# Performance work log

Hardware: AMD Instinct MI355X
Metric: run time of the kernel (lower is better)

The kernel has to match this reference:

```python
import jax, jax.numpy as jnp
import numpy as np
from jax import lax
import math

B, C, L, H, K, NCONV = 64, 128, 400, 8, 7, 4  # batch, d_model, length, n_head, kernel, n_conv
DK = C // H
EPS = 1e-5


def setup_inputs() -> dict:
    key = jax.random.key(0)
    ks = jax.random.split(key, 16)
    inp = {
        'x': jax.random.normal(ks[0], (B, C, L), dtype=jnp.float32),
        'mask': jnp.ones((B, L), dtype=jnp.float32),
        'dw_w': jax.random.normal(ks[1], (NCONV, C, 1, K), dtype=jnp.float32) * 0.1,
        'dw_b': jnp.zeros((NCONV, C), dtype=jnp.float32),
        'pw_w': jax.random.normal(ks[2], (NCONV, C, C, 1), dtype=jnp.float32) * 0.05,
        'pw_b': jnp.zeros((NCONV, C), dtype=jnp.float32),
        'wq': jax.random.normal(ks[3], (C, C), dtype=jnp.float32) * 0.05,
        'bq': jnp.zeros((C,), dtype=jnp.float32),
        'wk': jax.random.normal(ks[4], (C, C), dtype=jnp.float32) * 0.05,
        'bk': jnp.zeros((C,), dtype=jnp.float32),
        'wv': jax.random.normal(ks[5], (C, C), dtype=jnp.float32) * 0.05,
        'bv': jnp.zeros((C,), dtype=jnp.float32),
        'wo': jax.random.normal(ks[6], (C, C), dtype=jnp.float32) * 0.05,
        'bo': jnp.zeros((C,), dtype=jnp.float32),
        'fc_w': jax.random.normal(ks[7], (C, C), dtype=jnp.float32) * 0.05,
        'fc_b': jnp.zeros((C,), dtype=jnp.float32),
        'ln_g': jnp.ones((C, L), dtype=jnpp.float32) if False else jnp.ones((C, L), dtype=jnp.float32),
        'ln_b': jnp.zeros((C, L), dtype=jnp.float32),
    }
    return inp


def _pos_encoding():
    i = jnp.arange(C, dtype=jnp.float32)
    even = (jnp.arange(C) % 2) == 0
    freqs = jnp.where(even, 10000.0 ** (-i / C), -(10000.0 ** ((1.0 - i) / C)))
    phases = jnp.where(even, 0.0, math.pi / 2.0)
    pos = jnp.arange(L, dtype=jnp.float32)
    return jnp.sin(pos[None, :] * freqs[:, None] + phases[:, None])  # (C, L)


def _layer_norm(o, g, b):
    # torch LayerNorm([d_model, length]): normalize each sample over (C, L) jointly
    mu = jnp.mean(o, axis=(1, 2), keepdims=True)
    var = jnp.mean((o - mu) ** 2, axis=(1, 2), keepdims=True)
    return (o - mu) * lax.rsqrt(var + EPS) * g[None] + b[None]


def _dwsep_conv(o, dw, db, pw, pb):
    # depthwise: groups=C, kernel (C,1,K), 'same' padding
    y = lax.conv_general_dilated(o, dw, window_strides=(1,), padding=[(K // 2, K // 2)],
                                 dimension_numbers=('NCH', 'OIH', 'NCH'), feature_group_count=C)
    y = y + db[None, :, None]
    # pointwise 1x1 conv
    y = jnp.einsum('oc,bcl->bol', pw[:, :, 0], y) + pb[None, :, None]
    return y


def _attention(o, mask, wq, bq, wk, bk, wv, bv, wo, bo):
    xt = jnp.transpose(o, (0, 2, 1))  # (B, L, C)
    q = (xt @ wq.T + bq).reshape(B, L, H, DK)
    k = (xt @ wk.T + bk).reshape(B, L, H, DK)
    v = (xt @ wv.T + bv).reshape(B, L, H, DK)
    atten = jnp.einsum('blhd,bmhd->bhlm', q, k) / math.sqrt(C)  # note: sqrt(d_model), faithful
    m = mask[:, None, None, :]  # (B,1,1,L)
    atten = atten * m + (1.0 - m) * -1e30
    atten = jax.nn.softmax(atten, axis=-1)
    out = jnp.einsum('bhlm,bmhd->blhd', atten, v).reshape(B, L, C)
    out = out @ wo.T + bo
    return jnp.transpose(out, (0, 2, 1))  # (B, C, L)


def reference(x, mask, dw_w, dw_b, pw_w, pw_b, wq, bq, wk, bk, wv, bv, wo, bo, fc_w, fc_b, ln_g, ln_b):
    out = x + _pos_encoding()[None]
    res = out
    out = _layer_norm(out, ln_g, ln_b)
    for i in range(NCONV):
        out = _dwsep_conv(out, dw_w[i], dw_b[i], pw_w[i], pw_b[i])
        out = jax.nn.relu(out)
        out = res + out
        res = out
        out = _layer_norm(out, ln_g, ln_b)
    out = _attention(out, mask, wq, bq, wk, bk, wv, bv, wo, bo)
    out = res + out
    res = out
    out = _layer_norm(out, ln_g, ln_b)
    out = jnp.einsum('bcl,ec->bel', out, fc_w) + fc_b[None, :, None]
    out = jax.nn.relu(out)
    out = res + out
    return out
```

## Files before the change

kernel.cpp:

```cpp
#include <hip/hip_runtime.h>
#include <math.h>

constexpr int BN = 64;
constexpr int CC = 128;
constexpr int LL = 400;
constexpr int DK = 16;
constexpr int KK = 7;
constexpr int CL = CC * LL;
constexpr int NBCL = BN * CL;
constexpr float EPSV = 1e-5f;
constexpr float INV_N = 1.0f / (float)CL;
constexpr float BIGL = 1.4427e30f;
constexpr int RW = 96;

typedef __attribute__((ext_vector_type(8))) short bf16x8;
typedef __attribute__((ext_vector_type(4))) float f32x4;

#if defined(__has_builtin)
#if __has_builtin(__builtin_amdgcn_exp2f)
#define EXP2F(x) __builtin_amdgcn_exp2f(x)
#endif
#endif
#ifndef EXP2F
#define EXP2F(x) exp2f(x)
#endif

__device__ __forceinline__ short f2bf(float f) {
  unsigned u = __builtin_bit_cast(unsigned, f);
  u = (u + 0x7fffu + ((u >> 16) & 1u)) >> 16;
  return (short)u;
}
__device__ __forceinline__ float bf2f(unsigned short u) {
  return __builtin_bit_cast(float, (unsigned)u << 16);
}
__device__ __forceinline__ unsigned pkbf(float hi, float lo) {
  return __builtin_amdgcn_perm(__builtin_bit_cast(unsigned, hi),
                               __builtin_bit_cast(unsigned, lo), 0x07060302u);
}

__device__ __forceinline__ void stats_pub(float* sx, int u, int bb, int jx,
                                          float* red, int tid) {
  if (tid == 0) {
    float a = 0.f, b2 = 0.f;
    #pragma unroll
    for (int w2 = 0; w2 < 8; w2++) { a += red[w2 * 2]; b2 += red[w2 * 2 + 1]; }
    float* base = sx + (u * 64 + bb) * 32;
    __hip_atomic_store(&base[jx * 2], a, __ATOMIC_RELAXED, __HIP_MEMORY_SCOPE_AGENT);
    __hip_atomic_store(&base[jx * 2 + 1], b2, __ATOMIC_RELAXED, __HIP_MEMORY_SCOPE_AGENT);
    asm volatile("s_waitcnt vmcnt(0)" ::: "memory");
    __hip_atomic_fetch_add(reinterpret_cast<int*>(&base[16]), 1,
                           __ATOMIC_RELAXED, __HIP_MEMORY_SCOPE_AGENT);
  }
}
__device__ __forceinline__ void stats_wait(float* sx, int u, int bb,
                                           float* red, int tid,
                                           float& mu, float& rstd) {
  if (tid == 0) {
    float* base = sx + (u * 64 + bb) * 32;
    while (__hip_atomic_load(reinterpret_cast<int*>(&base[16]),
                             __ATOMIC_RELAXED, __HIP_MEMORY_SCOPE_AGENT) < 7)
      __builtin_amdgcn_s_sleep(1);
    float s1 = 0.f, s2 = 0.f;
    #pragma unroll
    for (int k = 0; k < 7; k++) {
      s1 += __hip_atomic_load(&base[k * 2], __ATOMIC_RELAXED, __HIP_MEMORY_SCOPE_AGENT);
      s2 += __hip_atomic_load(&base[k * 2 + 1], __ATOMIC_RELAXED, __HIP_MEMORY_SCOPE_AGENT);
    }
    float m2 = s1 * INV_N;
    red[0] = m2;
    red[1] = rsqrtf(s2 * INV_N - m2 * m2 + EPSV);
  }
  __syncthreads();
  mu = red[0]; rstd = red[1];
  __syncthreads();
}

template<int XMODE>
__device__ __forceinline__ void stage_x(
    short* __restrict__ XsF, const unsigned short* __restrict__ Xb,
    int j0, const float* __restrict__ lng, const float* __restrict__ lnb,
    float mu, float rstd, int tid)
{
  for (int idx = tid; idx < 1024; idx += 512) {
    int c = idx >> 3;
    int l8 = (idx & 7) * 8;
    int col0 = j0 + l8;
    short hv[8];
    bool valid = col0 < LL;
    int col0c = valid ? col0 : 0;
    const unsigned short* xp = Xb + c * LL + col0c;
    const ushort4 u0 = *reinterpret_cast<const ushort4*>(&xp[0]);
    const ushort4 u1 = *reinterpret_cast<const ushort4*>(&xp[4]);
    unsigned short uu[8] = {u0.x, u0.y, u0.z, u0.w, u1.x, u1.y, u1.z, u1.w};
    if (XMODE == 1) {
      #pragma unroll
      for (int e = 0; e < 8; e++) hv[e] = valid ? (short)uu[e] : (short)0;
    } else {
      const float* gp = lng + c * LL + col0c;
      const float* bp = lnb + c * LL + col0c;
      const float4 g0 = *reinterpret_cast<const float4*>(&gp[0]);
      const float4 g1 = *reinterpret_cast<const float4*>(&gp[4]);
      const float4 b0 = *reinterpret_cast<const float4*>(&bp[0]);
      const float4 b1 = *reinterpret_cast<const float4*>(&bp[4]);
      float gg[8] = {g0.x, g0.y, g0.z, g0.w, g1.x, g1.y, g1.z, g1.w};
      float bbv[8] = {b0.x, b0.y, b0.z, b0.w, b1.x, b1.y, b1.z, b1.w};
      #pragma unroll
      for (int e = 0; e < 8; e++) {
        float v = (bf2f(uu[e]) - mu) * rstd * gg[e] + bbv[e];
        hv[e] = valid ? f2bf(v) : (short)0;
      }
    }
    int t = (l8 >> 4) * 4 + (c >> 5);
    int quad = (c >> 3) & 3;
    int j = c & 7;
    int base = t * 512 + quad * 128 + j;
    int colb = l8 & 15;
    #pragma unroll
    for (int e = 0; e < 8; e++) XsF[base + (colb + e) * 8] = hv[e];
  }
}

template<int XMODE, int OMODE, bool RELU, bool ADDRES, bool STATS>
__device__ __forceinline__ void gemm_gl(
    short* __restrict__ XsF, float* __restrict__ red,
    const float* __restrict__ Wsrc, const unsigned short* __restrict__ Xv,
    const float* __restrict__ bias, const unsigned short* __restrict__ resid,
    const float* __restrict__ lng, const float* __restrict__ lnb,
    float mu, float rstd, void* __restrict__ Yv)
{
  int tid = threadIdx.x;
  int bb = blockIdx.y;
  int j0 = blockIdx.x * 64;
  int w = tid >> 6, lane = tid & 63;
  int o = w * 16 + (lane & 15);
  int cb = (lane >> 4) * 8;
  bf16x8 af[4];
  #pragma unroll
  for (int kt = 0; kt < 4; kt++) {
    const float* wp = Wsrc + o * 128 + kt * 32 + cb;
    const float4 a0 = *reinterpret_cast<const float4*>(wp);
    const float4 a1 = *reinterpret_cast<const float4*>(wp + 4);
    bf16x8 v;
    v[0] = f2bf(a0.x); v[1] = f2bf(a0.y); v[2] = f2bf(a0.z); v[3] = f2bf(a0.w);
    v[4] = f2bf(a1.x); v[5] = f2bf(a1.y); v[6] = f2bf(a1.z); v[7] = f2bf(a1.w);
    af[kt] = v;
  }
  stage_x<XMODE>(XsF, Xv + (size_t)bb * CL, j0, lng, lnb, mu, rstd, tid);
  __syncthreads();
  int col = lane & 15, quad = lane >> 4;
  f32x4 acc[4];
  #pragma unroll
  for (int lf = 0; lf < 4; lf++) acc[lf] = (f32x4){0.f, 0.f, 0.f, 0.f};
  #pragma unroll
  for (int kt = 0; kt < 4; kt++) {
    #pragma unroll
    for (int lf = 0; lf < 4; lf++) {
      bf16x8 bx = *reinterpret_cast<const bf16x8*>(&XsF[(lf * 4 + kt) * 512 + lane * 8]);
      acc[lf] = __builtin_amdgcn_mfma_f32_16x16x32_bf16(af[kt], bx, acc[lf], 0, 0, 0);
    }
  }
  int obase = w * 16;
  float bv[4];
  #pragma unroll
  for (int r = 0; r < 4; r++) bv[r] = bias[obase + quad * 4 + r];
  float lsum = 0.f, lsq = 0.f;
  #pragma unroll
  for (int lf = 0; lf < 4; lf++) {
    if (j0 + lf * 16 < LL) {
      int l = j0 + lf * 16 + col;
      #pragma unroll
      for (int r = 0; r < 4; r++) {
        float v = acc[lf][r] + bv[r];
        if (RELU) v = fmaxf(v, 0.f);
        size_t oidx = (size_t)bb * CL + (size_t)(obase + quad * 4 + r) * LL + l;
        if (ADDRES) v += bf2f(resid[oidx]);
        if (OMODE == 1) {
          unsigned short hb = (unsigned short)f2bf(v);
          ((unsigned short*)Yv)[oidx] = hb;
          if (STATS) { float vf = bf2f(hb); lsum += vf; lsq += vf * vf; }
        } else {
          ((float*)Yv)[oidx] = v;
        }
      }
    }
  }
  if (STATS) {
    #pragma unroll
    for (int off = 32; off > 0; off >>= 1) {
      lsum += __shfl_down(lsum, off);
      lsq  += __shfl_down(lsq, off);
    }
    if (lane == 0) { red[w * 2] = lsum; red[w * 2 + 1] = lsq; }
    __syncthreads();
  }
}

__global__ __launch_bounds__(512, 4) void fused_main(
    const float* __restrict__ pw_w, const float* __restrict__ wq,
    const float* __restrict__ wk, const float* __restrict__ wvp,
    const float* __restrict__ pw_b, const float* __restrict__ dw_b,
    const float* __restrict__ mask, const float* __restrict__ x,
    const float* __restrict__ lng, const float* __restrict__ lnb,
    const float* __restrict__ dw_w,
    const float* __restrict__ bq, const float* __restrict__ bk,
    const float* __restrict__ bvp,
    float* __restrict__ sx, float* __restrict__ maddb,
    unsigned short* __restrict__ r0,
    unsigned short* __restrict__ qt, unsigned short* __restrict__ kt,
    unsigned short* __restrict__ vbf)
{
  __shared__ short Raw[128 * RW];
  __shared__ short XsF[24 * 512];
  __shared__ float red[16];
  int tid = threadIdx.x;
  int jx = blockIdx.x, bb = blockIdx.y;
  int gtid = (bb * 7 + jx) * 512 + tid;
  int g0tile = jx * 64 - 16;

  if (gtid < 26624) {
    int b = gtid / 416, m = gtid - b * 416;
    maddb[gtid] = (m < LL) ? (mask[b * LL + m] - 1.f) * BIGL : -BIGL;
  }

  {
    float s1 = 0.f, s2 = 0.f;
    for (int idx = tid; idx < 1536; idx += 512) {
      int c = idx & 127, grp = idx >> 7;
      int r = grp * 8;
      float fc2 = (float)c, freq, ph;
      if ((c & 1) == 0) { freq = powf(10000.f, -fc2 / (float)CC);        ph = 0.f; }
      else              { freq = -powf(10000.f, (1.f - fc2) / (float)CC); ph = 1.5707963267948966f; }
      #pragma unroll
      for (int e4 = 0; e4 < 2; e4++) {
        int g = g0tile + r + e4 * 4;
        bool valid4 = (g >= 0) && (g <= LL - 4);
        float4 xv = {0.f, 0.f, 0.f, 0.f};
        if (valid4)
          xv = *reinterpret_cast<const float4*>(&x[((size_t)bb * CC + c) * LL + g]);
        float xe[4] = {xv.x, xv.y, xv.z, xv.w};
        #pragma unroll
        for (int e = 0; e < 4; e++) {
          int rr = r + e4 * 4 + e;
          short hh = 0;
          if (valid4) {
            float p = sinf((float)(g + e) * freq + ph);
            hh = f2bf(xe[e] + p);
          }
          Raw[c * RW + rr] = hh;
          if (rr >= 16 && rr < 80 && (g + e) < LL) {
            float v = bf2f((unsigned short)hh);
            s1 += v; s2 += v * v;
          }
        }
      }
    }
    #pragma unroll
    for (int off = 32; off > 0; off >>= 1) {
      s1 += __shfl_down(s1, off);
      s2 += __shfl_down(s2, off);
    }
    int wv = tid >> 6, lane = tid & 63;
    if (lane == 0) { red[wv * 2] = s1; red[wv * 2 + 1] = s2; }
    __syncthreads();
    stats_pub(sx, 0, bb, jx, red, tid);
  }

  int w = tid >> 6, lane = tid & 63;
  int col = lane & 15, quad = lane >> 4;
  int obase = w * 16;
  int wo_ = w * 16 + (lane & 15);
  int cb = (lane >> 4) * 8;
  #pragma unroll 1
  for (int li = 0; li < 4; li++) {
    float mu, rstd;
    stats_wait(sx, li, bb, red, tid, mu, rstd);
    const float* dww = dw_w + li * CC * KK;
    const float* dwb = dw_b + li * CC;
    for (int idx = tid; idx < 1536; idx += 512) {
      int c = idx & 127, grp = idx >> 7;
      int l8 = grp * 8;
      float xn[16];
      const float* gp = lng + c * LL;
      const float* bp = lnb + c * LL;
      #pragma unroll
      for (int g4 = 0; g4 < 4; g4++) {
        int r0w = l8 - 4 + g4 * 4;
        int rc = r0w < 0 ? 0 : (r0w > RW - 4 ? RW - 4 : r0w);
        const ushort4 rv = *reinterpret_cast<const ushort4*>(&Raw[c * RW + rc]);
        unsigned short rr4[4] = {rv.x, rv.y, rv.z, rv.w};
        int gg = g0tile + r0w;
        int ggc = gg < 0 ? 0 : (gg > LL - 4 ? LL - 4 : gg);
        const float4 gv = *reinterpret_cast<const float4*>(&gp[ggc]);
        const float4 bv4 = *reinterpret_cast<const float4*>(&bp[ggc]);
        float ge[4] = {gv.x, gv.y, gv.z, gv.w};
        float be[4] = {bv4.x, bv4.y, bv4.z, bv4.w};
        #pragma unroll
        for (int e = 0; e < 4; e++) {
          int g = gg + e;
          float v = (bf2f(rr4[e]) - mu) * rstd * ge[e] + be[e];
          xn[g4 * 4 + e] = (g >= 0 && g < LL) ? v : 0.f;
        }
      }
      float w7[KK];
      #pragma unroll
      for (int j = 0; j < KK; j++) w7[j] = dww[c * KK + j];
      float dbc = dwb[c];
      short hv[8];
      #pragma unroll
      for (int e = 0; e < 8; e++) {
        float a = 0.f;
        #pragma unroll
        for (int jj = 0; jj < KK; jj++) a += w7[jj] * xn[e + jj + 1];
        hv[e] = f2bf(a + dbc);
      }
      int t = (l8 >> 4) * 4 + (c >> 5);
      int qd = (c >> 3) & 3;
      int j = c & 7;
      int base = t * 512 + qd * 128 + j;
      int colb = l8 & 15;
      #pragma unroll
      for (int e = 0; e < 8; e++) XsF[base + (colb + e) * 8] = hv[e];
    }
    __syncthreads();
    const float* Wsrc = pw_w + li * 16384;
    bf16x8 af[4];
    #pragma unroll
    for (int kt = 0; kt < 4; kt++) {
      const float* wp = Wsrc + wo_ * 128 + kt * 32 + cb;
      const float4 a0 = *reinterpret_cast<const float4*>(wp);
      const float4 a1 = *reinterpret_cast<const float4*>(wp + 4);
      bf16x8 v;
      v[0] = f2bf(a0.x); v[1] = f2bf(a0.y); v[2] = f2bf(a0.z); v[3] = f2bf(a0.w);
      v[4] = f2bf(a1.x); v[5] = f2bf(a1.y); v[6] = f2bf(a1.z); v[7] = f2bf(a1.w);
      af[kt] = v;
    }
    f32x4 acc[6];
    #pragma unroll
    for (int lf = 0; lf < 6; lf++) acc[lf] = (f32x4){0.f, 0.f, 0.f, 0.f};
    #pragma unroll
    for (int kt = 0; kt < 4; kt++) {
      #pragma unroll
      for (int lf = 0; lf < 6; lf++) {
        bf16x8 bx = *reinterpret_cast<const bf16x8*>(&XsF[(lf * 4 + kt) * 512 + lane * 8]);
        acc[lf] = __builtin_amdgcn_mfma_f32_16x16x32_bf16(af[kt], bx, acc[lf], 0, 0, 0);
      }
    }
    const float* bias = pw_b + li * CC;
    float bv[4];
    #pragma unroll
    for (int r = 0; r < 4; r++) bv[r] = bias[obase + quad * 4 + r];
    int m = 12 - 4 * li;
    float lsum = 0.f, lsq = 0.f;
    #pragma unroll
    for (int lf = 0; lf < 6; lf++) {
      int r = lf * 16 + col;
      int g = g0tile + r;
      bool vcol = (r >= 16 - m) && (r < 80 + m) && (g >= 0) && (g < LL);
      #pragma unroll
      for (int rr = 0; rr < 4; rr++) {
        if (vcol) {
          int o = obase + quad * 4 + rr;
          float v = acc[lf][rr] + bv[rr];
          v = fmaxf(v, 0.f);
          v += bf2f((unsigned short)Raw[o * RW + r]);
          unsigned short hb = (unsigned short)f2bf(v);
          Raw[o * RW + r] = (short)hb;
          if (li == 3)
            r0[(size_t)bb * CL + (size_t)o * LL + g] = hb;
          if (r >= 16 && r < 80) {
            float vf = bf2f(hb);
            lsum += vf; lsq += vf * vf;
          }
        }
      }
    }
    #pragma unroll
    for (int off = 32; off > 0; off >>= 1) {
      lsum += __shfl_down(lsum, off);
      lsq  += __shfl_down(lsq, off);
    }
    if (lane == 0) { red[w * 2] = lsum; red[w * 2 + 1] = lsq; }
    __syncthreads();
    stats_pub(sx, li + 1, bb, jx, red, tid);
  }

  {
    float mu, rstd;
    stats_wait(sx, 4, bb, red, tid, mu, rstd);
    int j0 = jx * 64;
    for (int idx = tid; idx < 1024; idx += 512) {
      int c = idx >> 3;
      int l8 = (idx & 7) * 8;
      bool valid = (j0 + l8) < LL;
      short hv[8];
      const ushort4 u0 = *reinterpret_cast<const ushort4*>(&Raw[c * RW + 16 + l8]);
      const ushort4 u1 = *reinterpret_cast<const ushort4*>(&Raw[c * RW + 20 + l8]);
      unsigned short uu[8] = {u0.x, u0.y, u0.z, u0.w, u1.x, u1.y, u1.z, u1.w};
      int col0c = valid ? (j0 + l8) : 0;
      const float* gp = lng + c * LL + col0c;
      const float* bp = lnb + c * LL + col0c;
      const float4 g0 = *reinterpret_cast<const float4*>(&gp[0]);
      const float4 g1 = *reinterpret_cast<const float4*>(&gp[4]);
      const float4 b0 = *reinterpret_cast<const float4*>(&bp[0]);
      const float4 b1 = *reinterpret_cast<const float4*>(&bp[4]);
      float gg[8] = {g0.x, g0.y, g0.z, g0.w, g1.x, g1.y, g1.z, g1.w};
      float bbv[8] = {b0.x, b0.y, b0.z, b0.w, b1.x, b1.y, b1.z, b1.w};
      #pragma unroll
      for (int e = 0; e < 8; e++) {
        float v = (bf2f(uu[e]) - mu) * rstd * gg[e] + bbv[e];
        hv[e] = valid ? f2bf(v) : (short)0;
      }
      int t = (l8 >> 4) * 4 + (c >> 5);
      int qd = (c >> 3) & 3;
      int j = c & 7;
      int base = t * 512 + qd * 128 + j;
      int colb = l8 & 15;
      #pragma unroll
      for (int e = 0; e < 8; e++) XsF[base + (colb + e) * 8] = hv[e];
    }
    __syncthreads();
    int j0q = jx * 64;
    #pragma unroll 1
    for (int mm = 0; mm < 3; mm++) {
      const float* Wsrc = (mm == 0) ? wq : (mm == 1) ? wk : wvp;
      const float* bias = (mm == 0) ? bq : (mm == 1) ? bk : bvp;
      bf16x8 af[4];
      #pragma unroll
      for (int kt2 = 0; kt2 < 4; kt2++) {
        const float* wp = Wsrc + wo_ * 128 + kt2 * 32 + cb;
        const float4 a0 = *reinterpret_cast<const float4*>(wp);
        const float4 a1 = *reinterpret_cast<const float4*>(wp + 4);
        bf16x8 v;
        v[0] = f2bf(a0.x); v[1] = f2bf(a0.y); v[2] = f2bf(a0.z); v[3] = f2bf(a0.w);
        v[4] = f2bf(a1.x); v[5] = f2bf(a1.y); v[6] = f2bf(a1.z); v[7] = f2bf(a1.w);
        af[kt2] = v;
      }
      f32x4 acc[4];
      #pragma unroll
      for (int lf = 0; lf < 4; lf++) acc[lf] = (f32x4){0.f, 0.f, 0.f, 0.f};
      #pragma unroll
      for (int kt2 = 0; kt2 < 4; kt2++) {
        #pragma unroll
        for (int lf = 0; lf < 4; lf++) {
          bf16x8 bx = *reinterpret_cast<const bf16x8*>(&XsF[(lf * 4 + kt2) * 512 + lane * 8]);
          acc[lf] = __builtin_amdgcn_mfma_f32_16x16x32_bf16(af[kt2], bx, acc[lf], 0, 0, 0);
        }
      }
      float bv4[4];
      #pragma unroll
      for (int r = 0; r < 4; r++) bv4[r] = bias[obase + quad * 4 + r];
      if (mm < 2) {
        unsigned short* dst = (mm == 0) ? qt : kt;
        #pragma unroll
        for (int lf = 0; lf < 4; lf++) {
          if (j0q + lf * 16 < LL) {
            int l = j0q + lf * 16 + col;
            short4 hv4 = {f2bf(acc[lf][0] + bv4[0]), f2bf(acc[lf][1] + bv4[1]),
                          f2bf(acc[lf][2] + bv4[2]), f2bf(acc[lf][3] + bv4[3])};
            *reinterpret_cast<short4*>(
                &dst[(((size_t)bb * 8 + w) * LL + l) * 16 + quad * 4]) = hv4;
          }
        }
      } else {
        #pragma unroll
        for (int lf = 0; lf < 4; lf++) {
          if (j0q + lf * 16 < LL) {
            int l = j0q + lf * 16 + col;
            #pragma unroll
            for (int r = 0; r < 4; r++) {
              float v = acc[lf][r] + bv4[r];
              vbf[(size_t)bb * CL + (size_t)(obase + quad * 4 + r) * LL + l] =
                  (unsigned short)f2bf(v);
            }
          }
        }
      }
    }
  }
}

__global__ __launch_bounds__(512, 4) void wo_fc_fused(
    const float* __restrict__ wo, const float* __restrict__ fcw,
    const float* __restrict__ bo, const float* __restrict__ fcb,
    const unsigned short* __restrict__ tb,
    const unsigned short* __restrict__ r0, unsigned short* __restrict__ r1,
    const float* __restrict__ lng, const float* __restrict__ lnb,
    float* __restrict__ sx, float* __restrict__ out)
{
  __shared__ short XsF[16 * 512];
  __shared__ float red[16];
  int tid = threadIdx.x;
  int jx = blockIdx.x, bb = blockIdx.y;
  gemm_gl<1, 1, false, true, true>(XsF, red, wo, tb, bo, r0,
                                   nullptr, nullptr, 0.f, 0.f, r1);
  stats_pub(sx, 5, bb, jx, red, tid);
  float mu, rstd;
  stats_wait(sx, 5, bb, red, tid, mu, rstd);
  gemm_gl<0, 0, true, true, false>(XsF, red, fcw, r1, fcb, r1,
                                   lng, lnb, mu, rstd, out);
}

__global__ __launch_bounds__(256, 4) void attn_kernel(
    const unsigned short* __restrict__ qt, const unsigned short* __restrict__ kt,
    const unsigned short* __restrict__ vb, const float* __restrict__ maddb,
    unsigned short* __restrict__ ao)
{
  __shared__ short Pl[4][2][640];
  __shared__ float Mg[2][64][20];
  int bh = blockIdx.x;
  int b = bh >> 3, h = bh & 7;
  int w = threadIdx.x >> 6, lane = threadIdx.x & 63;
  int pair = w >> 1, half = w & 1;
  int tile = blockIdx.y * 2 + pair;
  bool live = tile < 7;
  int tile_c = live ? tile : 6;
  int col = lane & 15, quad = lane >> 4;
  int l0 = tile_c * 64;
  size_t trow = ((size_t)b * 8 + h) * LL;
  size_t base = ((size_t)b * CC + h * DK) * LL;
  const unsigned short* qp = qt + trow * 16;
  const unsigned short* kp = kt + trow * 16;
  const unsigned short* vp = vb + base;
  const float* mb = maddb + (size_t)b * 416;

  bf16x8 qf[4];
  #pragma unroll
  for (int f = 0; f < 4; f++) {
    bf16x8 v = {};
    if (quad < 2) {
      int l = l0 + f * 16 + col; int lc = l < LL ? l : LL - 1;
      v = *reinterpret_cast<const bf16x8*>(&qp[lc * 16 + quad * 8]);
    }
    qf[f] = v;
  }
  f32x4 of[4];
  float psum[4];
  #pragma unroll
  for (int f = 0; f < 4; f++) {
    of[f] = (f32x4){0.f, 0.f, 0.f, 0.f};
    psum[f] = 0.f;
  }
  const float scale2 = 0.08838834764831845f * 1.4426950408889634f;

  int mstart = half ? 224 : 0;
  int mend   = half ? 416 : 224;
  for (int m0 = mstart; m0 < mend; m0 += 32) {
    bf16x8 kf0 = {}, kf1 = {};
    if (quad < 2) {
      int mc0 = m0 + col < LL ? m0 + col : LL - 1;
      int mc1 = m0 + 16 + col < LL ? m0 + 16 + col : LL - 1;
      kf0 = *reinterpret_cast<const bf16x8*>(&kp[mc0 * 16 + quad * 8]);
      kf1 = *reinterpret_cast<const bf16x8*>(&kp[mc1 * 16 + quad * 8]);
    }
    bf16x8 vf;
    {
      int ms = m0 + quad * 8; if (ms > LL - 8) ms = LL - 8;
      vf = *reinterpret_cast<const bf16x8*>(&vp[col * LL + ms]);
    }
    const float4 a4 = *reinterpret_cast<const float4*>(&mb[m0 + quad * 4]);
    const float4 b4 = *reinterpret_cast<const float4*>(&mb[m0 + 16 + quad * 4]);
    float madd[8] = {a4.x, a4.y, a4.z, a4.w, b4.x, b4.y, b4.z, b4.w};
    #pragma unroll
    for (int f = 0; f < 4; f++) {
      f32x4 z = {0.f, 0.f, 0.f, 0.f};
      f32x4 s0 = __builtin_amdgcn_mfma_f32_16x16x32_bf16(kf0, qf[f], z, 0, 0, 0);
      f32x4 s1 = __builtin_amdgcn_mfma_f32_16x16x32_bf16(kf1, qf[f], z, 0, 0, 0);
      float p[8];
      #pragma unroll
      for (int r = 0; r < 4; r++) {
        p[r]     = EXP2F(s0[r] * scale2 + madd[r]);
        p[4 + r] = EXP2F(s1[r] * scale2 + madd[4 + r]);
      }
      float ps = 0.f;
      #pragma unroll
      for (int i = 0; i < 8; i++) ps += p[i];
      psum[f] += ps;
      short* row = &Pl[w][f & 1][col * 40];
      short4 h0 = __builtin_bit_cast(short4, make_uint2(pkbf(p[1], p[0]), pkbf(p[3], p[2])));
      short4 h1 = __builtin_bit_cast(short4, make_uint2(pkbf(p[5], p[4]), pkbf(p[7], p[6])));
      *reinterpret_cast<short4*>(&row[quad * 4])      = h0;
      *reinterpret_cast<short4*>(&row[16 + quad * 4]) = h1;
      bf16x8 pf = *reinterpret_cast<const bf16x8*>(&Pl[w][f & 1][col * 40 + quad * 8]);
      of[f] = __builtin_amdgcn_mfma_f32_16x16x32_bf16(vf, pf, of[f], 0, 0, 0);
    }
  }
  if (half == 1) {
    float* mg = &Mg[pair][lane][0];
    #pragma unroll
    for (int f = 0; f < 4; f++) {
      #pragma unroll
      for (int r = 0; r < 4; r++) mg[f * 4 + r] = of[f][r];
      mg[16 + f] = psum[f];
    }
  }
  __syncthreads();
  if (half == 0 && live) {
    const float* mg = &Mg[pair][lane][0];
    #pragma unroll
    for (int f = 0; f < 4; f++) {
      #pragma unroll
      for (int r = 0; r < 4; r++) of[f][r] += mg[f * 4 + r];
      psum[f] += mg[16 + f];
    }
    #pragma unroll
    for (int f = 0; f < 4; f++) {
      float s = psum[f];
      s += __shfl_xor(s, 16);
      s += __shfl_xor(s, 32);
      float inv = 1.f / s;
      int lf = l0 + f * 16;
      if (lf < LL) {
        #pragma unroll
        for (int r = 0; r < 4; r++)
          ao[base + (size_t)(quad * 4 + r) * LL + lf + col] =
              (unsigned short)f2bf(of[f][r] * inv);
      }
    }
  }
}

extern "C" void kernel_launch(void* const* d_in, const int* in_sizes, int n_in,
                              void* d_out, int out_size, void* d_ws, size_t ws_size,
                              hipStream_t stream) {
  const float* x    = (const float*)d_in[0];
  const float* mask = (const float*)d_in[1];
  const float* dw_w = (const float*)d_in[2];
  const float* dw_b = (const float*)d_in[3];
  const float* pw_w = (const float*)d_in[4];
  const float* pw_b = (const float*)d_in[5];
  const float* wq   = (const float*)d_in[6];
  const float* bq   = (const float*)d_in[7];
  const float* wk   = (const float*)d_in[8];
  const float* bk   = (const float*)d_in[9];
  const float* wvp  = (const float*)d_in[10];
  const float* bv   = (const float*)d_in[11];
  const float* wo   = (const float*)d_in[12];
  const float* bo   = (const float*)d_in[13];
  const float* fcw  = (const float*)d_in[14];
  const float* fcb  = (const float*)d_in[15];
  const float* lng  = (const float*)d_in[16];
  const float* lnb  = (const float*)d_in[17];
  float* out = (float*)d_out;
  float* ws  = (float*)d_ws;

  float* sx    = ws;
  float* maddb = ws + 6 * 64 * 32;
  unsigned short* r0 = (unsigned short*)(maddb + 64 * 416);
  unsigned short* r1 = r0 + NBCL;
  unsigned short* qt = r1 + NBCL;
  unsigned short* kt = qt + NBCL;
  unsigned short* vbf = kt + NBCL;
  unsigned short* tb = vbf + NBCL;

  hipMemsetAsync(sx, 0, 6 * 64 * 32 * sizeof(float), stream);

  fused_main<<<dim3(7, BN), 512, 0, stream>>>(
      pw_w, wq, wk, wvp, pw_b, dw_b, mask, x, lng, lnb, dw_w,
      bq, bk, bv, sx, maddb, r0, qt, kt, vbf);
  attn_kernel<<<dim3(512, 4), 256, 0, stream>>>(qt, kt, vbf, maddb, tb);
  wo_fc_fused<<<dim3(7, BN), 512, 0, stream>>>(
      wo, fcw, bo, fcb, tb, r0, r1, lng, lnb, sx, out);
}
```

Before: 248.6 us.

## Fuse attention into the Wo/FC kernel and keep intermediates in shared memory

Merges the separate attention kernel into the Wo projection, LayerNorm and FC kernel. Each 512-thread block handles one 64-column tile of one batch, with one wave per head running the full key loop instead of splitting keys across two waves. The attention output and the post-Wo residual r1 now stay in LDS rather than going through global buffers, which removes a kernel launch and global round trips. In exchange the grid drops to 448 blocks from 2048 smaller attention blocks, each wave's key loop doubles in length, and the Raw row stride is padded to 100, likely to reduce LDS bank conflicts.

```diff
diff --git a/kernel.cpp b/kernel.cpp
--- a/kernel.cpp
+++ b/kernel.cpp
@@ -11,7 +11,7 @@
 constexpr float EPSV = 1e-5f;
 constexpr float INV_N = 1.0f / (float)CL;
 constexpr float BIGL = 1.4427e30f;
-constexpr int RW = 96;
+constexpr int RW = 100;
 
 typedef __attribute__((ext_vector_type(8))) short bf16x8;
 typedef __attribute__((ext_vector_type(4))) float f32x4;
@@ -73,126 +73,6 @@
   __syncthreads();
   mu = red[0]; rstd = red[1];
   __syncthreads();
-}
-
-template<int XMODE>
-__device__ __forceinline__ void stage_x(
-    short* __restrict__ XsF, const unsigned short* __restrict__ Xb,
-    int j0, const float* __restrict__ lng, const float* __restrict__ lnb,
-    float mu, float rstd, int tid)
-{
-  for (int idx = tid; idx < 1024; idx += 512) {
-    int c = idx >> 3;
-    int l8 = (idx & 7) * 8;
-    int col0 = j0 + l8;
-    short hv[8];
-    bool valid = col0 < LL;
-    int col0c = valid ? col0 : 0;
-    const unsigned short* xp = Xb + c * LL + col0c;
-    const ushort4 u0 = *reinterpret_cast<const ushort4*>(&xp[0]);
-    const ushort4 u1 = *reinterpret_cast<const ushort4*>(&xp[4]);
-    unsigned short uu[8] = {u0.x, u0.y, u0.z, u0.w, u1.x, u1.y, u1.z, u1.w};
-    if (XMODE == 1) {
-      #pragma unroll
-      for (int e = 0; e < 8; e++) hv[e] = valid ? (short)uu[e] : (short)0;
-    } else {
-      const float* gp = lng + c * LL + col0c;
-      const float* bp = lnb + c * LL + col0c;
-      const float4 g0 = *reinterpret_cast<const float4*>(&gp[0]);
-      const float4 g1 = *reinterpret_cast<const float4*>(&gp[4]);
-      const float4 b0 = *reinterpret_cast<const float4*>(&bp[0]);
-      const float4 b1 = *reinterpret_cast<const float4*>(&bp[4]);
-      float gg[8] = {g0.x, g0.y, g0.z, g0.w, g1.x, g1.y, g1.z, g1.w};
-      float bbv[8] = {b0.x, b0.y, b0.z, b0.w, b1.x, b1.y, b1.z, b1.w};
-      #pragma unroll
-      for (int e = 0; e < 8; e++) {
-        float v = (bf2f(uu[e]) - mu) * rstd * gg[e] + bbv[e];
-        hv[e] = valid ? f2bf(v) : (short)0;
-      }
-    }
-    int t = (l8 >> 4) * 4 + (c >> 5);
-    int quad = (c >> 3) & 3;
-    int j = c & 7;
-    int base = t * 512 + quad * 128 + j;
-    int colb = l8 & 15;
-    #pragma unroll
-    for (int e = 0; e < 8; e++) XsF[base + (colb + e) * 8] = hv[e];
-  }
-}
-
-template<int XMODE, int OMODE, bool RELU, bool ADDRES, bool STATS>
-__device__ __forceinline__ void gemm_gl(
-    short* __restrict__ XsF, float* __restrict__ red,
-    const float* __restrict__ Wsrc, const unsigned short* __restrict__ Xv,
-    const float* __restrict__ bias, const unsigned short* __restrict__ resid,
-    const float* __restrict__ lng, const float* __restrict__ lnb,
-    float mu, float rstd, void* __restrict__ Yv)
-{
-  int tid = threadIdx.x;
-  int bb = blockIdx.y;
-  int j0 = blockIdx.x * 64;
-  int w = tid >> 6, lane = tid & 63;
-  int o = w * 16 + (lane & 15);
-  int cb = (lane >> 4) * 8;
-  bf16x8 af[4];
-  #pragma unroll
-  for (int kt = 0; kt < 4; kt++) {
-    const float* wp = Wsrc + o * 128 + kt * 32 + cb;
-    const float4 a0 = *reinterpret_cast<const float4*>(wp);
-    const float4 a1 = *reinterpret_cast<const float4*>(wp + 4);
-    bf16x8 v;
-    v[0] = f2bf(a0.x); v[1] = f2bf(a0.y); v[2] = f2bf(a0.z); v[3] = f2bf(a0.w);
-    v[4] = f2bf(a1.x); v[5] = f2bf(a1.y); v[6] = f2bf(a1.z); v[7] = f2bf(a1.w);
-    af[kt] = v;
-  }
-  stage_x<XMODE>(XsF, Xv + (size_t)bb * CL, j0, lng, lnb, mu, rstd, tid);
-  __syncthreads();
-  int col = lane & 15, quad = lane >> 4;
-  f32x4 acc[4];
-  #pragma unroll
-  for (int lf = 0; lf < 4; lf++) acc[lf] = (f32x4){0.f, 0.f, 0.f, 0.f};
-  #pragma unroll
-  for (int kt = 0; kt < 4; kt++) {
-    #pragma unroll
-    for (int lf = 0; lf < 4; lf++) {
-      bf16x8 bx = *reinterpret_cast<const bf16x8*>(&XsF[(lf * 4 + kt) * 512 + lane * 8]);
-      acc[lf] = __builtin_amdgcn_mfma_f32_16x16x32_bf16(af[kt], bx, acc[lf], 0, 0, 0);
-    }
-  }
-  int obase = w * 16;
-  float bv[4];
-  #pragma unroll
-  for (int r = 0; r < 4; r++) bv[r] = bias[obase + quad * 4 + r];
-  float lsum = 0.f, lsq = 0.f;
-  #pragma unroll
-  for (int lf = 0; lf < 4; lf++) {
-    if (j0 + lf * 16 < LL) {
-      int l = j0 + lf * 16 + col;
-      #pragma unroll
-      for (int r = 0; r < 4; r++) {
-        float v = acc[lf][r] + bv[r];
-        if (RELU) v = fmaxf(v, 0.f);
-        size_t oidx = (size_t)bb * CL + (size_t)(obase + quad * 4 + r) * LL + l;
-        if (ADDRES) v += bf2f(resid[oidx]);
-        if (OMODE == 1) {
-          unsigned short hb = (unsigned short)f2bf(v);
-          ((unsigned short*)Yv)[oidx] = hb;
-          if (STATS) { float vf = bf2f(hb); lsum += vf; lsq += vf * vf; }
-        } else {
-          ((float*)Yv)[oidx] = v;
-        }
-      }
-    }
-  }
-  if (STATS) {
-    #pragma unroll
-    for (int off = 32; off > 0; off >>= 1) {
-      lsum += __shfl_down(lsum, off);
-      lsq  += __shfl_down(lsq, off);
-    }
-    if (lane == 0) { red[w * 2] = lsum; red[w * 2 + 1] = lsq; }
-    __syncthreads();
-  }
 }
 
 __global__ __launch_bounds__(512, 4) void fused_main(
@@ -285,7 +165,7 @@
       #pragma unroll
       for (int g4 = 0; g4 < 4; g4++) {
         int r0w = l8 - 4 + g4 * 4;
-        int rc = r0w < 0 ? 0 : (r0w > RW - 4 ? RW - 4 : r0w);
+        int rc = r0w < 0 ? 0 : (r0w > 96 - 4 ? 96 - 4 : r0w);
         const ushort4 rv = *reinterpret_cast<const ushort4*>(&Raw[c * RW + rc]);
         unsigned short rr4[4] = {rv.x, rv.y, rv.z, rv.w};
         int gg = g0tile + r0w;
@@ -479,49 +359,31 @@
   }
 }
 
-__global__ __launch_bounds__(512, 4) void wo_fc_fused(
+__global__ __launch_bounds__(512, 4) void attn_wo_fc(
+    const unsigned short* __restrict__ qt, const unsigned short* __restrict__ kt,
+    const unsigned short* __restrict__ vbf, const float* __restrict__ maddb,
+    const unsigned short* __restrict__ r0,
     const float* __restrict__ wo, const float* __restrict__ fcw,
     const float* __restrict__ bo, const float* __restrict__ fcb,
-    const unsigned short* __restrict__ tb,
-    const unsigned short* __restrict__ r0, unsigned short* __restrict__ r1,
     const float* __restrict__ lng, const float* __restrict__ lnb,
     float* __restrict__ sx, float* __restrict__ out)
 {
+  __shared__ short Pl[8][2][640];
   __shared__ short XsF[16 * 512];
+  __shared__ short R1[128 * 68];
   __shared__ float red[16];
   int tid = threadIdx.x;
   int jx = blockIdx.x, bb = blockIdx.y;
-  gemm_gl<1, 1, false, true, true>(XsF, red, wo, tb, bo, r0,
-                                   nullptr, nullptr, 0.f, 0.f, r1);
-  stats_pub(sx, 5, bb, jx, red, tid);
-  float mu, rstd;
-  stats_wait(sx, 5, bb, red, tid, mu, rstd);
-  gemm_gl<0, 0, true, true, false>(XsF, red, fcw, r1, fcb, r1,
-                                   lng, lnb, mu, rstd, out);
-}
-
-__global__ __launch_bounds__(256, 4) void attn_kernel(
-    const unsigned short* __restrict__ qt, const unsigned short* __restrict__ kt,
-    const unsigned short* __restrict__ vb, const float* __restrict__ maddb,
-    unsigned short* __restrict__ ao)
-{
-  __shared__ short Pl[4][2][640];
-  __shared__ float Mg[2][64][20];
-  int bh = blockIdx.x;
-  int b = bh >> 3, h = bh & 7;
-  int w = threadIdx.x >> 6, lane = threadIdx.x & 63;
-  int pair = w >> 1, half = w & 1;
-  int tile = blockIdx.y * 2 + pair;
-  bool live = tile < 7;
-  int tile_c = live ? tile : 6;
+  int w = tid >> 6, lane = tid & 63;
+  int h = w;
   int col = lane & 15, quad = lane >> 4;
-  int l0 = tile_c * 64;
-  size_t trow = ((size_t)b * 8 + h) * LL;
-  size_t base = ((size_t)b * CC + h * DK) * LL;
+  int l0 = jx * 64;
+  size_t trow = ((size_t)bb * 8 + h) * LL;
   const unsigned short* qp = qt + trow * 16;
   const unsigned short* kp = kt + trow * 16;
-  const unsigned short* vp = vb + base;
-  const float* mb = maddb + (size_t)b * 416;
+  const unsigned short* vp = vbf + ((size_t)bb * CC + h * DK) * LL;
+  const float* mb = maddb + (size_t)bb * 416;
+  const float scale2 = 0.08838834764831845f * 1.4426950408889634f;
 
   bf16x8 qf[4];
   #pragma unroll
@@ -540,11 +402,7 @@
     of[f] = (f32x4){0.f, 0.f, 0.f, 0.f};
     psum[f] = 0.f;
   }
-  const float scale2 = 0.08838834764831845f * 1.4426950408889634f;
-
-  int mstart = half ? 224 : 0;
-  int mend   = half ? 416 : 224;
-  for (int m0 = mstart; m0 < mend; m0 += 32) {
+  for (int m0 = 0; m0 < 416; m0 += 32) {
     bf16x8 kf0 = {}, kf1 = {};
     if (quad < 2) {
       int mc0 = m0 + col < LL ? m0 + col : LL - 1;
@@ -584,36 +442,150 @@
       of[f] = __builtin_amdgcn_mfma_f32_16x16x32_bf16(vf, pf, of[f], 0, 0, 0);
     }
   }
-  if (half == 1) {
-    float* mg = &Mg[pair][lane][0];
-    #pragma unroll
-    for (int f = 0; f < 4; f++) {
-      #pragma unroll
-      for (int r = 0; r < 4; r++) mg[f * 4 + r] = of[f][r];
-      mg[16 + f] = psum[f];
+  #pragma unroll
+  for (int f = 0; f < 4; f++) {
+    float s = psum[f];
+    s += __shfl_xor(s, 16);
+    s += __shfl_xor(s, 32);
+    float inv = 1.f / s;
+    if (l0 + f * 16 < LL) {
+      #pragma unroll
+      for (int r = 0; r < 4; r++) {
+        int c = h * 16 + quad * 4 + r;
+        short vv = f2bf(of[f][r] * inv);
+        XsF[(f * 4 + (c >> 5)) * 512 + ((c >> 3) & 3) * 128 + (c & 7) + col * 8] = vv;
+      }
     }
   }
   __syncthreads();
-  if (half == 0 && live) {
-    const float* mg = &Mg[pair][lane][0];
-    #pragma unroll
-    for (int f = 0; f < 4; f++) {
-      #pragma unroll
-      for (int r = 0; r < 4; r++) of[f][r] += mg[f * 4 + r];
-      psum[f] += mg[16 + f];
-    }
-    #pragma unroll
-    for (int f = 0; f < 4; f++) {
-      float s = psum[f];
-      s += __shfl_xor(s, 16);
-      s += __shfl_xor(s, 32);
-      float inv = 1.f / s;
-      int lf = l0 + f * 16;
-      if (lf < LL) {
-        #pragma unroll
-        for (int r = 0; r < 4; r++)
-          ao[base + (size_t)(quad * 4 + r) * LL + lf + col] =
-              (unsigned short)f2bf(of[f][r] * inv);
+
+  int obase = w * 16;
+  int wo_ = w * 16 + (lane & 15);
+  int cb = (lane >> 4) * 8;
+  {
+    bf16x8 af[4];
+    #pragma unroll
+    for (int kt2 = 0; kt2 < 4; kt2++) {
+      const float* wp = wo + wo_ * 128 + kt2 * 32 + cb;
+      const float4 a0 = *reinterpret_cast<const float4*>(wp);
+      const float4 a1 = *reinterpret_cast<const float4*>(wp + 4);
+      bf16x8 v;
+      v[0] = f2bf(a0.x); v[1] = f2bf(a0.y); v[2] = f2bf(a0.z); v[3] = f2bf(a0.w);
+      v[4] = f2bf(a1.x); v[5] = f2bf(a1.y); v[6] = f2bf(a1.z); v[7] = f2bf(a1.w);
+      af[kt2] = v;
+    }
+    f32x4 acc[4];
+    #pragma unroll
+    for (int lf = 0; lf < 4; lf++) acc[lf] = (f32x4){0.f, 0.f, 0.f, 0.f};
+    #pragma unroll
+    for (int kt2 = 0; kt2 < 4; kt2++) {
+      #pragma unroll
+      for (int lf = 0; lf < 4; lf++) {
+        bf16x8 bx = *reinterpret_cast<const bf16x8*>(&XsF[(lf * 4 + kt2) * 512 + lane * 8]);
+        acc[lf] = __builtin_amdgcn_mfma_f32_16x16x32_bf16(af[kt2], bx, acc[lf], 0, 0, 0);
+      }
+    }
+    float bv4[4];
+    #pragma unroll
+    for (int r = 0; r < 4; r++) bv4[r] = bo[obase + quad * 4 + r];
+    float lsum = 0.f, lsq = 0.f;
+    #pragma unroll
+    for (int lf = 0; lf < 4; lf++) {
+      if (l0 + lf * 16 < LL) {
+        int l = l0 + lf * 16 + col;
+        #pragma unroll
+        for (int r = 0; r < 4; r++) {
+          int o = obase + quad * 4 + r;
+          float v = acc[lf][r] + bv4[r];
+          v += bf2f(r0[(size_t)bb * CL + (size_t)o * LL + l]);
+          unsigned short hb = (unsigned short)f2bf(v);
+          R1[o * 68 + lf * 16 + col] = (short)hb;
+          float vf = bf2f(hb);
+          lsum += vf; lsq += vf * vf;
+        }
+      }
+    }
+    #pragma unroll
+    for (int off = 32; off > 0; off >>= 1) {
+      lsum += __shfl_down(lsum, off);
+      lsq  += __shfl_down(lsq, off);
+    }
+    if (lane == 0) { red[w * 2] = lsum; red[w * 2 + 1] = lsq; }
+    __syncthreads();
+    stats_pub(sx, 5, bb, jx, red, tid);
+  }
+
+  {
+    float mu, rstd;
+    stats_wait(sx, 5, bb, red, tid, mu, rstd);
+    for (int idx = tid; idx < 1024; idx += 512) {
+      int c = idx >> 3;
+      int l8 = (idx & 7) * 8;
+      bool valid = (l0 + l8) < LL;
+      short hv[8];
+      const ushort4 u0 = *reinterpret_cast<const ushort4*>(&R1[c * 68 + l8]);
+      const ushort4 u1 = *reinterpret_cast<const ushort4*>(&R1[c * 68 + l8 + 4]);
+      unsigned short uu[8] = {u0.x, u0.y, u0.z, u0.w, u1.x, u1.y, u1.z, u1.w};
+      int col0c = valid ? (l0 + l8) : 0;
+      const float* gp = lng + c * LL + col0c;
+      const float* bp = lnb + c * LL + col0c;
+      const float4 g0 = *reinterpret_cast<const float4*>(&gp[0]);
+      const float4 g1 = *reinterpret_cast<const float4*>(&gp[4]);
+      const float4 b0 = *reinterpret_cast<const float4*>(&bp[0]);
+      const float4 b1 = *reinterpret_cast<const float4*>(&bp[4]);
+      float gg[8] = {g0.x, g0.y, g0.z, g0.w, g1.x, g1.y, g1.z, g1.w};
+      float bbv[8] = {b0.x, b0.y, b0.z, b0.w, b1.x, b1.y, b1.z, b1.w};
+      #pragma unroll
+      for (int e = 0; e < 8; e++) {
+        float v = (bf2f(uu[e]) - mu) * rstd * gg[e] + bbv[e];
+        hv[e] = valid ? f2bf(v) : (short)0;
+      }
+      int t = (l8 >> 4) * 4 + (c >> 5);
+      int qd = (c >> 3) & 3;
+      int j = c & 7;
+      int base = t * 512 + qd * 128 + j;
+      int colb = l8 & 15;
+      #pragma unroll
+      for (int e = 0; e < 8; e++) XsF[base + (colb + e) * 8] = hv[e];
+    }
+    __syncthreads();
+    bf16x8 af[4];
+    #pragma unroll
+    for (int kt2 = 0; kt2 < 4; kt2++) {
+      const float* wp = fcw + wo_ * 128 + kt2 * 32 + cb;
+      const float4 a0 = *reinterpret_cast<const float4*>(wp);
+      const float4 a1 = *reinterpret_cast<const float4*>(wp + 4);
+      bf16x8 v;
+      v[0] = f2bf(a0.x); v[1] = f2bf(a0.y); v[2] = f2bf(a0.z); v[3] = f2bf(a0.w);
+      v[4] = f2bf(a1.x); v[5] = f2bf(a1.y); v[6] = f2bf(a1.z); v[7] = f2bf(a1.w);
+      af[kt2] = v;
+    }
+    f32x4 acc[4];
+    #pragma unroll
+    for (int lf = 0; lf < 4; lf++) acc[lf] = (f32x4){0.f, 0.f, 0.f, 0.f};
+    #pragma unroll
+    for (int kt2 = 0; kt2 < 4; kt2++) {
+      #pragma unroll
+      for (int lf = 0; lf < 4; lf++) {
+        bf16x8 bx = *reinterpret_cast<const bf16x8*>(&XsF[(lf * 4 + kt2) * 512 + lane * 8]);
+        acc[lf] = __builtin_amdgcn_mfma_f32_16x16x32_bf16(af[kt2], bx, acc[lf], 0, 0, 0);
+      }
+    }
+    float bv4[4];
+    #pragma unroll
+    for (int r = 0; r < 4; r++) bv4[r] = fcb[obase + quad * 4 + r];
+    #pragma unroll
+    for (int lf = 0; lf < 4; lf++) {
+      if (l0 + lf * 16 < LL) {
+        int l = l0 + lf * 16 + col;
+        #pragma unroll
+        for (int r = 0; r < 4; r++) {
+          int o = obase + quad * 4 + r;
+          float v = acc[lf][r] + bv4[r];
+          v = fmaxf(v, 0.f);
+          v += bf2f((unsigned short)R1[o * 68 + lf * 16 + col]);
+          out[(size_t)bb * CL + (size_t)o * LL + l] = v;
+        }
       }
     }
   }
@@ -646,18 +618,15 @@
   float* sx    = ws;
   float* maddb = ws + 6 * 64 * 32;
   unsigned short* r0 = (unsigned short*)(maddb + 64 * 416);
-  unsigned short* r1 = r0 + NBCL;
-  unsigned short* qt = r1 + NBCL;
+  unsigned short* qt = r0 + NBCL;
   unsigned short* kt = qt + NBCL;
   unsigned short* vbf = kt + NBCL;
-  unsigned short* tb = vbf + NBCL;
 
   hipMemsetAsync(sx, 0, 6 * 64 * 32 * sizeof(float), stream);
 
   fused_main<<<dim3(7, BN), 512, 0, stream>>>(
       pw_w, wq, wk, wvp, pw_b, dw_b, mask, x, lng, lnb, dw_w,
       bq, bk, bv, sx, maddb, r0, qt, kt, vbf);
-  attn_kernel<<<dim3(512, 4), 256, 0, stream>>>(qt, kt, vbf, maddb, tb);
-  wo_fc_fused<<<dim3(7, BN), 512, 0, stream>>>(
-      wo, fcw, bo, fcb, tb, r0, r1, lng, lnb, sx, out);
-}
+  attn_wo_fc<<<dim3(7, BN), 512, 0, stream>>>(
+      qt, kt, vbf, maddb, r0, wo, fcw, bo, fcb, lng, lnb, sx, out);
+}
```

New measurement: 240.7 us. 1.03x faster.
